# Performance work log

Hardware: AMD Instinct MI355X
Metric: run time of the kernel (lower is better)

Reference implementation:

```python
import jax, jax.numpy as jnp
import numpy as np

N_NODES = 100000
N_EDGES = 3200000
F_IN = 512
HIDDEN = 16
N_CLASSES = 16


def setup_inputs() -> dict:
    key = jax.random.key(0)
    k1, k2, k3, k4 = jax.random.split(key, 4)
    x = jax.random.normal(k1, (N_NODES, F_IN), dtype=jnp.float32)
    edge_index = jax.random.randint(k2, (2, N_EDGES), 0, N_NODES, dtype=jnp.int32)
    # Glorot-style init for GCN weights
    W1 = jax.random.normal(k3, (F_IN, HIDDEN), dtype=jnp.float32) * np.float32(np.sqrt(2.0 / (F_IN + HIDDEN)))
    b1 = jnp.zeros((HIDDEN,), dtype=jnp.float32)
    W2 = jax.random.normal(k4, (HIDDEN, N_CLASSES), dtype=jnp.float32) * np.float32(np.sqrt(2.0 / (HIDDEN + N_CLASSES)))
    b2 = jnp.zeros((N_CLASSES,), dtype=jnp.float32)
    return {"x": x, "W1": W1, "b1": b1, "W2": W2, "b2": b2, "edge_index": edge_index}


def _gcn_conv(x, src, dst, W, b, n_nodes):
    """PyG GCNConv: h = x @ W, then symmetric-normalized aggregation with self-loops, + bias."""
    h = x @ W  # [N, out]
    # degrees include self-loops (edge weight 1.0 everywhere)
    ones = jnp.ones(src.shape[0], dtype=h.dtype)
    deg = jax.ops.segment_sum(ones, dst, num_segments=n_nodes) + 1.0  # +1 for self-loop
    dinv = jax.lax.rsqrt(deg)  # deg >= 1, no zero guard needed
    norm = dinv[src] * dinv[dst]  # [E]
    agg = jax.ops.segment_sum(h[src] * norm[:, None], dst, num_segments=n_nodes)
    # self-loop contribution: norm_ii = 1/deg_i
    agg = agg + h * (dinv * dinv)[:, None]
    return agg + b


def reference(x, W1, b1, W2, b2, edge_index):
    src, dst = edge_index[0], edge_index[1]
    n = x.shape[0]
    h = jax.nn.relu(_gcn_conv(x, src, dst, W1, b1, n))
    # dropout is identity in eval mode
    out = _gcn_conv(h, src, dst, W2, b2, n)
    return jax.nn.log_softmax(out, axis=1)
```

## Files before the change

kernel.cpp:

```cpp
#include <hip/hip_runtime.h>
#include <hip/hip_bf16.h>
#include <math.h>

constexpr int N_NODES = 100000;
constexpr int N_EDGES = 3200000;
constexpr int F_IN    = 512;
constexpr int HID     = 16;

constexpr int NPAD = 100352;

constexpr int B_BITS = 8;
constexpr int NPB    = 1 << B_BITS;
constexpr int NBKT   = (N_NODES + NPB - 1) / NPB;
constexpr int SBLK   = 400;
constexpr int CHUNK  = N_EDGES / SBLK;
constexpr int CAP    = 10240;

typedef float f32x4 __attribute__((ext_vector_type(4)));
typedef short bfrag8 __attribute__((ext_vector_type(8)));

__device__ __forceinline__ unsigned short f2bf_rne(float f) {
    unsigned int u = __float_as_uint(f);
    u += 0x7FFFu + ((u >> 16) & 1u);
    return (unsigned short)(u >> 16);
}
__device__ __forceinline__ float bf2f(unsigned short u) {
    return __uint_as_float((unsigned int)u << 16);
}

__global__ __launch_bounds__(256) void prep_kernel(const float* __restrict__ W1,
                                                   unsigned short* __restrict__ w1t,
                                                   int* __restrict__ gcur,
                                                   unsigned short* __restrict__ hh_bf,
                                                   unsigned short* __restrict__ hh2_bf) {
    int i = blockIdx.x * 256 + threadIdx.x;
    if (i < F_IN * HID) {
        int k = i >> 4, n = i & 15;
        w1t[n * F_IN + k] = f2bf_rne(W1[i]);
    }
    if (i < NBKT) gcur[i] = i * CAP;
    if (i < 16) {
        hh_bf [N_NODES * 16 + i] = 0;
        hh2_bf[N_NODES * 16 + i] = 0;
    }
}

__global__ __launch_bounds__(1024) void bin_scatter_kernel(const int* __restrict__ src,
                                                           const int* __restrict__ dst,
                                                           int* __restrict__ gcur,
                                                           unsigned int* __restrict__ binned) {
    __shared__ int sdst[CHUNK];
    __shared__ int ssrc[CHUNK];
    __shared__ int cnt[NBKT];
    __shared__ int cur[NBKT];
    const int tid = threadIdx.x;
    for (int t = tid; t < NBKT; t += 1024) cnt[t] = 0;
    const int base = blockIdx.x * CHUNK;
    for (int i = tid; i < CHUNK; i += 1024) {
        sdst[i] = dst[base + i];
        ssrc[i] = src[base + i];
    }
    __syncthreads();
    for (int i = tid; i < CHUNK; i += 1024)
        atomicAdd(&cnt[sdst[i] >> B_BITS], 1);
    __syncthreads();
    for (int t = tid; t < NBKT; t += 1024)
        cur[t] = cnt[t] ? atomicAdd(&gcur[t], cnt[t]) : 0;
    __syncthreads();
    for (int i = tid; i < CHUNK; i += 1024) {
        int d = sdst[i];
        int b = d >> B_BITS;
        int pos = atomicAdd(&cur[b], 1);
        binned[pos] = ((unsigned)(d & (NPB - 1)) << 24) | (unsigned)ssrc[i];
    }
}

__global__ __launch_bounds__(1024) void csr_bucket_kernel(const unsigned int* __restrict__ binned,
                                                          const int* __restrict__ gcur,
                                                          int2* __restrict__ row2,
                                                          int* __restrict__ csr,
                                                          float* __restrict__ dinv) {
    __shared__ unsigned int eb[CAP];
    __shared__ int deg[NPB];
    __shared__ int pre[NPB];
    __shared__ int cur[NPB];
    const int tid = threadIdx.x;
    const int b = blockIdx.x;
    const int e0 = b * CAP;
    int ne = gcur[b] - e0;
    if (ne > CAP) ne = CAP;
    if (ne < 0) ne = 0;

    if (tid < NPB) deg[tid] = 0;
    for (int i = tid; i < ne; i += 1024) eb[i] = binned[e0 + i];
    __syncthreads();
    for (int i = tid; i < ne; i += 1024)
        atomicAdd(&deg[eb[i] >> 24], 1);
    __syncthreads();
    if (tid < NPB) pre[tid] = (deg[tid] + 3) & ~3;
    __syncthreads();
    for (int off = 1; off < NPB; off <<= 1) {
        int v = 0;
        if (tid < NPB && tid >= off) v = pre[tid - off];
        __syncthreads();
        if (tid < NPB) pre[tid] += v;
        __syncthreads();
    }
    if (tid < NPB) {
        int excl = (tid == 0) ? 0 : pre[tid - 1];
        int start = e0 + excl;
        cur[tid] = start;
        int node = b * NPB + tid;
        if (node < N_NODES) {
            int pd = (deg[tid] + 3) & ~3;
            row2[node] = make_int2(start, start + pd);
            dinv[node] = rsqrtf((float)deg[tid] + 1.0f);
        }
    }
    __syncthreads();
    for (int i = tid; i < ne; i += 1024) {
        unsigned int v = eb[i];
        int pos = atomicAdd(&cur[v >> 24], 1);
        csr[pos] = (int)(v & 0xFFFFFFu);
    }
    if (tid < NPB) {
        int node = b * NPB + tid;
        if (node < N_NODES) {
            int d = deg[tid];
            int pdl = (d + 3) & ~3;
            int s = e0 + ((tid == 0) ? 0 : pre[tid - 1]) + d;
            for (int q = d; q < pdl; ++q) csr[s++] = N_NODES;
        }
    }
}

__global__ __launch_bounds__(256) void gemm1_kernel(const float* __restrict__ x,
                                                    const unsigned short* __restrict__ w1t,
                                                    const float* __restrict__ b1,
                                                    const float* __restrict__ dinv,
                                                    unsigned short* __restrict__ hh_bf,
                                                    float* __restrict__ aggs1) {
    const int tid  = threadIdx.x;
    const int lane = tid & 63;
    const int wv   = tid >> 6;
    const int m    = lane & 15;
    const int quad = lane >> 4;
    const int node0 = blockIdx.x * 64 + wv * 16;

    int gm = node0 + m; if (gm >= N_NODES) gm = N_NODES - 1;
    const float* arow = x + (size_t)gm * F_IN + quad * 8;

    bfrag8 bfr[16];
    const unsigned short* wbase = w1t + m * F_IN + quad * 8;
    #pragma unroll
    for (int t = 0; t < 16; ++t)
        bfr[t] = *(const bfrag8*)(wbase + t * 32);

    f32x4 acc = {0.f, 0.f, 0.f, 0.f};
    #pragma unroll 4
    for (int t = 0; t < 16; ++t) {
        float4 lo = *(const float4*)(arow + t * 32);
        float4 hi = *(const float4*)(arow + t * 32 + 4);
        union { bfrag8 fr; __hip_bfloat162 h2[4]; } u;
        u.h2[0] = __float22bfloat162_rn(float2{lo.x, lo.y});
        u.h2[1] = __float22bfloat162_rn(float2{lo.z, lo.w});
        u.h2[2] = __float22bfloat162_rn(float2{hi.x, hi.y});
        u.h2[3] = __float22bfloat162_rn(float2{hi.z, hi.w});
        acc = __builtin_amdgcn_mfma_f32_16x16x32_bf16(u.fr, bfr[t], acc, 0, 0, 0);
    }

    const float b1j = b1[m];
    #pragma unroll
    for (int r = 0; r < 4; ++r) {
        int gn = node0 + quad * 4 + r;
        if (gn < N_NODES) {
            float dv = dinv[gn];
            float hv = acc[r] * dv;
            size_t o = (size_t)gn * 16 + m;
            hh_bf[o] = f2bf_rne(hv);
            aggs1[o] = hv * dv + b1j;
        }
    }
}

__global__ __launch_bounds__(256) void pull1_kernel(const unsigned short* __restrict__ hh_bf,
                                                    const float* __restrict__ aggs1,
                                                    const float* __restrict__ dinv,
                                                    const int2* __restrict__ row2,
                                                    const int* __restrict__ csr,
                                                    const float* __restrict__ W2,
                                                    const float* __restrict__ b2,
                                                    unsigned short* __restrict__ hh2_bf,
                                                    float* __restrict__ aggs2) {
    __shared__ f32x4 w2s[64];
    __shared__ f32x4 b2s[4];
    const int tid = threadIdx.x;
    if (tid < 64) w2s[tid] = ((const f32x4*)W2)[tid];
    if (tid < 4)  b2s[tid] = ((const f32x4*)b2)[tid];
    __syncthreads();

    int t = blockIdx.x * 256 + tid;
    int node = t >> 2;
    int l = t & 3;
    if (node >= N_NODES) return;

    int2 re = row2[node];
    int p = re.x, e = re.y;
    const unsigned short* hb = hh_bf + (l << 2);
    f32x4 a0 = {0,0,0,0}, a1 = {0,0,0,0}, a2 = {0,0,0,0}, a3 = {0,0,0,0};
    f32x4 a4 = {0,0,0,0}, a5 = {0,0,0,0}, a6 = {0,0,0,0}, a7 = {0,0,0,0};
    for (; p + 8 <= e; p += 8) {
        int4 sA = *(const int4*)(csr + p);
        int4 sB = *(const int4*)(csr + p + 4);
        ushort4 g0 = *(const ushort4*)(hb + (sA.x << 4));
        ushort4 g1 = *(const ushort4*)(hb + (sA.y << 4));
        ushort4 g2 = *(const ushort4*)(hb + (sA.z << 4));
        ushort4 g3 = *(const ushort4*)(hb + (sA.w << 4));
        ushort4 g4 = *(const ushort4*)(hb + (sB.x << 4));
        ushort4 g5 = *(const ushort4*)(hb + (sB.y << 4));
        ushort4 g6 = *(const ushort4*)(hb + (sB.z << 4));
        ushort4 g7 = *(const ushort4*)(hb + (sB.w << 4));
        a0.x += bf2f(g0.x); a0.y += bf2f(g0.y); a0.z += bf2f(g0.z); a0.w += bf2f(g0.w);
        a1.x += bf2f(g1.x); a1.y += bf2f(g1.y); a1.z += bf2f(g1.z); a1.w += bf2f(g1.w);
        a2.x += bf2f(g2.x); a2.y += bf2f(g2.y); a2.z += bf2f(g2.z); a2.w += bf2f(g2.w);
        a3.x += bf2f(g3.x); a3.y += bf2f(g3.y); a3.z += bf2f(g3.z); a3.w += bf2f(g3.w);
        a4.x += bf2f(g4.x); a4.y += bf2f(g4.y); a4.z += bf2f(g4.z); a4.w += bf2f(g4.w);
        a5.x += bf2f(g5.x); a5.y += bf2f(g5.y); a5.z += bf2f(g5.z); a5.w += bf2f(g5.w);
        a6.x += bf2f(g6.x); a6.y += bf2f(g6.y); a6.z += bf2f(g6.z); a6.w += bf2f(g6.w);
        a7.x += bf2f(g7.x); a7.y += bf2f(g7.y); a7.z += bf2f(g7.z); a7.w += bf2f(g7.w);
    }
    if (p < e) {
        int4 s = *(const int4*)(csr + p);
        ushort4 g0 = *(const ushort4*)(hb + (s.x << 4));
        ushort4 g1 = *(const ushort4*)(hb + (s.y << 4));
        ushort4 g2 = *(const ushort4*)(hb + (s.z << 4));
        ushort4 g3 = *(const ushort4*)(hb + (s.w << 4));
        a0.x += bf2f(g0.x); a0.y += bf2f(g0.y); a0.z += bf2f(g0.z); a0.w += bf2f(g0.w);
        a1.x += bf2f(g1.x); a1.y += bf2f(g1.y); a1.z += bf2f(g1.z); a1.w += bf2f(g1.w);
        a2.x += bf2f(g2.x); a2.y += bf2f(g2.y); a2.z += bf2f(g2.z); a2.w += bf2f(g2.w);
        a3.x += bf2f(g3.x); a3.y += bf2f(g3.y); a3.z += bf2f(g3.z); a3.w += bf2f(g3.w);
    }
    f32x4 a = ((a0 + a1) + (a2 + a3)) + ((a4 + a5) + (a6 + a7));
    float dv = dinv[node];
    f32x4 base = *(const f32x4*)(aggs1 + ((size_t)node << 4) + (l << 2));
    float v[4];
    #pragma unroll
    for (int c = 0; c < 4; ++c) v[c] = fmaxf(base[c] + dv * a[c], 0.f);

    f32x4 h2 = {0.f, 0.f, 0.f, 0.f};
    #pragma unroll
    for (int k = 0; k < 16; ++k) {
        float vk = __shfl(v[k & 3], k >> 2, 4);
        f32x4 w = w2s[k * 4 + l];
        h2.x += vk * w.x; h2.y += vk * w.y; h2.z += vk * w.z; h2.w += vk * w.w;
    }
    f32x4 bb = b2s[l];
    ushort4 hs;
    f32x4 ag;
    float hv0 = h2.x * dv; hs.x = f2bf_rne(hv0); ag.x = hv0 * dv + bb.x;
    float hv1 = h2.y * dv; hs.y = f2bf_rne(hv1); ag.y = hv1 * dv + bb.y;
    float hv2 = h2.z * dv; hs.z = f2bf_rne(hv2); ag.z = hv2 * dv + bb.z;
    float hv3 = h2.w * dv; hs.w = f2bf_rne(hv3); ag.w = hv3 * dv + bb.w;
    size_t o = ((size_t)node << 4) + (l << 2);
    *(ushort4*)(hh2_bf + o) = hs;
    *(f32x4*)(aggs2 + o) = ag;
}

__global__ __launch_bounds__(256) void pull2_kernel(const unsigned short* __restrict__ hh2_bf,
                                                    const float* __restrict__ aggs2,
                                                    const float* __restrict__ dinv,
                                                    const int2* __restrict__ row2,
                                                    const int* __restrict__ csr,
                                                    float* __restrict__ out) {
    int t = blockIdx.x * 256 + threadIdx.x;
    int node = t >> 2;
    int l = t & 3;
    if (node >= N_NODES) return;

    int2 re = row2[node];
    int p = re.x, e = re.y;
    const unsigned short* hb = hh2_bf + (l << 2);
    f32x4 a0 = {0,0,0,0}, a1 = {0,0,0,0}, a2 = {0,0,0,0}, a3 = {0,0,0,0};
    f32x4 a4 = {0,0,0,0}, a5 = {0,0,0,0}, a6 = {0,0,0,0}, a7 = {0,0,0,0};
    for (; p + 8 <= e; p += 8) {
        int4 sA = *(const int4*)(csr + p);
        int4 sB = *(const int4*)(csr + p + 4);
        ushort4 g0 = *(const ushort4*)(hb + (sA.x << 4));
        ushort4 g1 = *(const ushort4*)(hb + (sA.y << 4));
        ushort4 g2 = *(const ushort4*)(hb + (sA.z << 4));
        ushort4 g3 = *(const ushort4*)(hb + (sA.w << 4));
        ushort4 g4 = *(const ushort4*)(hb + (sB.x << 4));
        ushort4 g5 = *(const ushort4*)(hb + (sB.y << 4));
        ushort4 g6 = *(const ushort4*)(hb + (sB.z << 4));
        ushort4 g7 = *(const ushort4*)(hb + (sB.w << 4));
        a0.x += bf2f(g0.x); a0.y += bf2f(g0.y); a0.z += bf2f(g0.z); a0.w += bf2f(g0.w);
        a1.x += bf2f(g1.x); a1.y += bf2f(g1.y); a1.z += bf2f(g1.z); a1.w += bf2f(g1.w);
        a2.x += bf2f(g2.x); a2.y += bf2f(g2.y); a2.z += bf2f(g2.z); a2.w += bf2f(g2.w);
        a3.x += bf2f(g3.x); a3.y += bf2f(g3.y); a3.z += bf2f(g3.z); a3.w += bf2f(g3.w);
        a4.x += bf2f(g4.x); a4.y += bf2f(g4.y); a4.z += bf2f(g4.z); a4.w += bf2f(g4.w);
        a5.x += bf2f(g5.x); a5.y += bf2f(g5.y); a5.z += bf2f(g5.z); a5.w += bf2f(g5.w);
        a6.x += bf2f(g6.x); a6.y += bf2f(g6.y); a6.z += bf2f(g6.z); a6.w += bf2f(g6.w);
        a7.x += bf2f(g7.x); a7.y += bf2f(g7.y); a7.z += bf2f(g7.z); a7.w += bf2f(g7.w);
    }
    if (p < e) {
        int4 s = *(const int4*)(csr + p);
        ushort4 g0 = *(const ushort4*)(hb + (s.x << 4));
        ushort4 g1 = *(const ushort4*)(hb + (s.y << 4));
        ushort4 g2 = *(const ushort4*)(hb + (s.z << 4));
        ushort4 g3 = *(const ushort4*)(hb + (s.w << 4));
        a0.x += bf2f(g0.x); a0.y += bf2f(g0.y); a0.z += bf2f(g0.z); a0.w += bf2f(g0.w);
        a1.x += bf2f(g1.x); a1.y += bf2f(g1.y); a1.z += bf2f(g1.z); a1.w += bf2f(g1.w);
        a2.x += bf2f(g2.x); a2.y += bf2f(g2.y); a2.z += bf2f(g2.z); a2.w += bf2f(g2.w);
        a3.x += bf2f(g3.x); a3.y += bf2f(g3.y); a3.z += bf2f(g3.z); a3.w += bf2f(g3.w);
    }
    f32x4 a = ((a0 + a1) + (a2 + a3)) + ((a4 + a5) + (a6 + a7));
    float dv = dinv[node];
    f32x4 base = *(const f32x4*)(aggs2 + ((size_t)node << 4) + (l << 2));
    f32x4 o4;
    o4.x = base.x + dv * a.x; o4.y = base.y + dv * a.y;
    o4.z = base.z + dv * a.z; o4.w = base.w + dv * a.w;

    float m = fmaxf(fmaxf(o4.x, o4.y), fmaxf(o4.z, o4.w));
    m = fmaxf(m, __shfl_xor(m, 1));
    m = fmaxf(m, __shfl_xor(m, 2));
    float s = expf(o4.x - m) + expf(o4.y - m) + expf(o4.z - m) + expf(o4.w - m);
    s += __shfl_xor(s, 1);
    s += __shfl_xor(s, 2);
    float ls = m + logf(s);
    f32x4 r;
    r.x = o4.x - ls; r.y = o4.y - ls; r.z = o4.z - ls; r.w = o4.w - ls;
    *(f32x4*)(out + ((size_t)node << 4) + (l << 2)) = r;
}

extern "C" void kernel_launch(void* const* d_in, const int* in_sizes, int n_in,
                              void* d_out, int out_size, void* d_ws, size_t ws_size,
                              hipStream_t stream) {
    const float* x    = (const float*)d_in[0];
    const float* W1   = (const float*)d_in[1];
    const float* b1   = (const float*)d_in[2];
    const float* W2   = (const float*)d_in[3];
    const float* b2   = (const float*)d_in[4];
    const int*   ei   = (const int*)d_in[5];
    const int*   src  = ei;
    const int*   dst  = ei + N_EDGES;
    float* out = (float*)d_out;

    constexpr size_t SLOTS    = (size_t)NBKT * CAP;
    constexpr size_t OFF_DINV = 512;
    constexpr size_t OFF_ROW2 = 512 + (size_t)NPAD;
    constexpr size_t OFF_CSR  = 512 + 3 * (size_t)NPAD;
    constexpr size_t OFF_HH   = OFF_CSR + SLOTS;
    constexpr size_t OFF_AG1  = OFF_HH + 800512;
    constexpr size_t OFF_HH2  = OFF_AG1 + 1600000;
    constexpr size_t OFF_AG2  = OFF_HH2 + 800512;
    constexpr size_t OFF_W1T  = OFF_AG2 + 1600000;

    int*   wsi  = (int*)d_ws;
    float* wsf  = (float*)d_ws;
    int*   gcur  = wsi;
    float* dinv  = wsf + OFF_DINV;
    int2*  row2  = (int2*)(wsi + OFF_ROW2);
    int*   csr   = wsi + OFF_CSR;
    unsigned int* binned = (unsigned int*)csr;
    unsigned short* hh_bf  = (unsigned short*)(wsi + OFF_HH);
    float*          aggs1  = wsf + OFF_AG1;
    unsigned short* hh2_bf = (unsigned short*)(wsi + OFF_HH2);
    float*          aggs2  = wsf + OFF_AG2;
    unsigned short* w1t    = (unsigned short*)(wsi + OFF_W1T);

    const int MB  = (N_NODES + 63) / 64;
    const int GB4 = (N_NODES * 4 + 255) / 256;

    prep_kernel       <<<32, 256, 0, stream>>>(W1, w1t, gcur, hh_bf, hh2_bf);
    bin_scatter_kernel<<<SBLK, 1024, 0, stream>>>(src, dst, gcur, binned);
    csr_bucket_kernel <<<NBKT, 1024, 0, stream>>>(binned, gcur, row2, csr, dinv);
    gemm1_kernel      <<<MB, 256, 0, stream>>>(x, w1t, b1, dinv, hh_bf, aggs1);
    pull1_kernel      <<<GB4, 256, 0, stream>>>(hh_bf, aggs1, dinv, row2, csr, W2, b2, hh2_bf, aggs2);
    pull2_kernel      <<<GB4, 256, 0, stream>>>(hh2_bf, aggs2, dinv, row2, csr, out);
}
```

Measured before the change: 437.8 us.

## Split edges across quad lanes with full-row gathers and shuffle reduction

```diff
diff --git a/kernel.cpp b/kernel.cpp
--- a/kernel.cpp
+++ b/kernel.cpp
@@ -17,6 +17,8 @@
 constexpr int CAP    = 10240;
 
 typedef float f32x4 __attribute__((ext_vector_type(4)));
+typedef float f32x8 __attribute__((ext_vector_type(8)));
+typedef unsigned short u16x8 __attribute__((ext_vector_type(8)));
 typedef short bfrag8 __attribute__((ext_vector_type(8)));
 
 __device__ __forceinline__ unsigned short f2bf_rne(float f) {
@@ -183,6 +185,55 @@
     }
 }
 
+__device__ __forceinline__ f32x4 gather_rows_reduce(const unsigned short* __restrict__ tbl,
+                                                    const int* __restrict__ csr,
+                                                    int p, int e, int l) {
+    f32x8 pA0 = {0,0,0,0,0,0,0,0}, pB0 = {0,0,0,0,0,0,0,0};
+    f32x8 pA1 = {0,0,0,0,0,0,0,0}, pB1 = {0,0,0,0,0,0,0,0};
+    for (; p + 4 < e; p += 8) {
+        int s0 = csr[p];
+        int s1 = csr[p + 4];
+        const unsigned short* r0 = tbl + (s0 << 4);
+        const unsigned short* r1 = tbl + (s1 << 4);
+        u16x8 a0 = *(const u16x8*)(r0);
+        u16x8 b0 = *(const u16x8*)(r0 + 8);
+        u16x8 a1 = *(const u16x8*)(r1);
+        u16x8 b1 = *(const u16x8*)(r1 + 8);
+        #pragma unroll
+        for (int c = 0; c < 8; ++c) {
+            pA0[c] += bf2f(a0[c]); pB0[c] += bf2f(b0[c]);
+            pA1[c] += bf2f(a1[c]); pB1[c] += bf2f(b1[c]);
+        }
+    }
+    if (p < e) {
+        int s0 = csr[p];
+        const unsigned short* r0 = tbl + (s0 << 4);
+        u16x8 a0 = *(const u16x8*)(r0);
+        u16x8 b0 = *(const u16x8*)(r0 + 8);
+        #pragma unroll
+        for (int c = 0; c < 8; ++c) {
+            pA0[c] += bf2f(a0[c]); pB0[c] += bf2f(b0[c]);
+        }
+    }
+    f32x8 A = pA0 + pA1;
+    f32x8 B = pB0 + pB1;
+    const bool hi2 = (l & 2) != 0;
+    f32x8 send = hi2 ? A : B;
+    f32x8 keep = hi2 ? B : A;
+    #pragma unroll
+    for (int c = 0; c < 8; ++c) keep[c] += __shfl_xor(send[c], 2);
+    const bool hi1 = (l & 1) != 0;
+    f32x4 s2, k2;
+    #pragma unroll
+    for (int c = 0; c < 4; ++c) {
+        s2[c] = hi1 ? keep[c] : keep[c + 4];
+        k2[c] = hi1 ? keep[c + 4] : keep[c];
+    }
+    #pragma unroll
+    for (int c = 0; c < 4; ++c) k2[c] += __shfl_xor(s2[c], 1);
+    return k2;
+}
+
 __global__ __launch_bounds__(256) void pull1_kernel(const unsigned short* __restrict__ hh_bf,
                                                     const float* __restrict__ aggs1,
                                                     const float* __restrict__ dinv,
@@ -205,42 +256,8 @@
     if (node >= N_NODES) return;
 
     int2 re = row2[node];
-    int p = re.x, e = re.y;
-    const unsigned short* hb = hh_bf + (l << 2);
-    f32x4 a0 = {0,0,0,0}, a1 = {0,0,0,0}, a2 = {0,0,0,0}, a3 = {0,0,0,0};
-    f32x4 a4 = {0,0,0,0}, a5 = {0,0,0,0}, a6 = {0,0,0,0}, a7 = {0,0,0,0};
-    for (; p + 8 <= e; p += 8) {
-        int4 sA = *(const int4*)(csr + p);
-        int4 sB = *(const int4*)(csr + p + 4);
-        ushort4 g0 = *(const ushort4*)(hb + (sA.x << 4));
-        ushort4 g1 = *(const ushort4*)(hb + (sA.y << 4));
-        ushort4 g2 = *(const ushort4*)(hb + (sA.z << 4));
-        ushort4 g3 = *(const ushort4*)(hb + (sA.w << 4));
-        ushort4 g4 = *(const ushort4*)(hb + (sB.x << 4));
-        ushort4 g5 = *(const ushort4*)(hb + (sB.y << 4));
-        ushort4 g6 = *(const ushort4*)(hb + (sB.z << 4));
-        ushort4 g7 = *(const ushort4*)(hb + (sB.w << 4));
-        a0.x += bf2f(g0.x); a0.y += bf2f(g0.y); a0.z += bf2f(g0.z); a0.w += bf2f(g0.w);
-        a1.x += bf2f(g1.x); a1.y += bf2f(g1.y); a1.z += bf2f(g1.z); a1.w += bf2f(g1.w);
-        a2.x += bf2f(g2.x); a2.y += bf2f(g2.y); a2.z += bf2f(g2.z); a2.w += bf2f(g2.w);
-        a3.x += bf2f(g3.x); a3.y += bf2f(g3.y); a3.z += bf2f(g3.z); a3.w += bf2f(g3.w);
-        a4.x += bf2f(g4.x); a4.y += bf2f(g4.y); a4.z += bf2f(g4.z); a4.w += bf2f(g4.w);
-        a5.x += bf2f(g5.x); a5.y += bf2f(g5.y); a5.z += bf2f(g5.z); a5.w += bf2f(g5.w);
-        a6.x += bf2f(g6.x); a6.y += bf2f(g6.y); a6.z += bf2f(g6.z); a6.w += bf2f(g6.w);
-        a7.x += bf2f(g7.x); a7.y += bf2f(g7.y); a7.z += bf2f(g7.z); a7.w += bf2f(g7.w);
-    }
-    if (p < e) {
-        int4 s = *(const int4*)(csr + p);
-        ushort4 g0 = *(const ushort4*)(hb + (s.x << 4));
-        ushort4 g1 = *(const ushort4*)(hb + (s.y << 4));
-        ushort4 g2 = *(const ushort4*)(hb + (s.z << 4));
-        ushort4 g3 = *(const ushort4*)(hb + (s.w << 4));
-        a0.x += bf2f(g0.x); a0.y += bf2f(g0.y); a0.z += bf2f(g0.z); a0.w += bf2f(g0.w);
-        a1.x += bf2f(g1.x); a1.y += bf2f(g1.y); a1.z += bf2f(g1.z); a1.w += bf2f(g1.w);
-        a2.x += bf2f(g2.x); a2.y += bf2f(g2.y); a2.z += bf2f(g2.z); a2.w += bf2f(g2.w);
-        a3.x += bf2f(g3.x); a3.y += bf2f(g3.y); a3.z += bf2f(g3.z); a3.w += bf2f(g3.w);
-    }
-    f32x4 a = ((a0 + a1) + (a2 + a3)) + ((a4 + a5) + (a6 + a7));
+    f32x4 a = gather_rows_reduce(hh_bf, csr, re.x + l, re.y, l);
+
     float dv = dinv[node];
     f32x4 base = *(const f32x4*)(aggs1 + ((size_t)node << 4) + (l << 2));
     float v[4];
@@ -278,42 +295,8 @@
     if (node >= N_NODES) return;
 
     int2 re = row2[node];
-    int p = re.x, e = re.y;
-    const unsigned short* hb = hh2_bf + (l << 2);
-    f32x4 a0 = {0,0,0,0}, a1 = {0,0,0,0}, a2 = {0,0,0,0}, a3 = {0,0,0,0};
-    f32x4 a4 = {0,0,0,0}, a5 = {0,0,0,0}, a6 = {0,0,0,0}, a7 = {0,0,0,0};
-    for (; p + 8 <= e; p += 8) {
-        int4 sA = *(const int4*)(csr + p);
-        int4 sB = *(const int4*)(csr + p + 4);
-        ushort4 g0 = *(const ushort4*)(hb + (sA.x << 4));
-        ushort4 g1 = *(const ushort4*)(hb + (sA.y << 4));
-        ushort4 g2 = *(const ushort4*)(hb + (sA.z << 4));
-        ushort4 g3 = *(const ushort4*)(hb + (sA.w << 4));
-        ushort4 g4 = *(const ushort4*)(hb + (sB.x << 4));
-        ushort4 g5 = *(const ushort4*)(hb + (sB.y << 4));
-        ushort4 g6 = *(const ushort4*)(hb + (sB.z << 4));
-        ushort4 g7 = *(const ushort4*)(hb + (sB.w << 4));
-        a0.x += bf2f(g0.x); a0.y += bf2f(g0.y); a0.z += bf2f(g0.z); a0.w += bf2f(g0.w);
-        a1.x += bf2f(g1.x); a1.y += bf2f(g1.y); a1.z += bf2f(g1.z); a1.w += bf2f(g1.w);
-        a2.x += bf2f(g2.x); a2.y += bf2f(g2.y); a2.z += bf2f(g2.z); a2.w += bf2f(g2.w);
-        a3.x += bf2f(g3.x); a3.y += bf2f(g3.y); a3.z += bf2f(g3.z); a3.w += bf2f(g3.w);
-        a4.x += bf2f(g4.x); a4.y += bf2f(g4.y); a4.z += bf2f(g4.z); a4.w += bf2f(g4.w);
-        a5.x += bf2f(g5.x); a5.y += bf2f(g5.y); a5.z += bf2f(g5.z); a5.w += bf2f(g5.w);
-        a6.x += bf2f(g6.x); a6.y += bf2f(g6.y); a6.z += bf2f(g6.z); a6.w += bf2f(g6.w);
-        a7.x += bf2f(g7.x); a7.y += bf2f(g7.y); a7.z += bf2f(g7.z); a7.w += bf2f(g7.w);
-    }
-    if (p < e) {
-        int4 s = *(const int4*)(csr + p);
-        ushort4 g0 = *(const ushort4*)(hb + (s.x << 4));
-        ushort4 g1 = *(const ushort4*)(hb + (s.y << 4));
-        ushort4 g2 = *(const ushort4*)(hb + (s.z << 4));
-        ushort4 g3 = *(const ushort4*)(hb + (s.w << 4));
-        a0.x += bf2f(g0.x); a0.y += bf2f(g0.y); a0.z += bf2f(g0.z); a0.w += bf2f(g0.w);
-        a1.x += bf2f(g1.x); a1.y += bf2f(g1.y); a1.z += bf2f(g1.z); a1.w += bf2f(g1.w);
-        a2.x += bf2f(g2.x); a2.y += bf2f(g2.y); a2.z += bf2f(g2.z); a2.w += bf2f(g2.w);
-        a3.x += bf2f(g3.x); a3.y += bf2f(g3.y); a3.z += bf2f(g3.z); a3.w += bf2f(g3.w);
-    }
-    f32x4 a = ((a0 + a1) + (a2 + a3)) + ((a4 + a5) + (a6 + a7));
+    f32x4 a = gather_rows_reduce(hh2_bf, csr, re.x + l, re.y, l);
+
     float dv = dinv[node];
     f32x4 base = *(const f32x4*)(aggs2 + ((size_t)node << 4) + (l << 2));
     f32x4 o4;
```

Measured after the change: 448.2 us. 2.4% more time.
